# Kernel optimization log

Hardware: AMD Instinct MI355X
Metric: run time of the kernel (lower is better)

## Reference

```python
import jax, jax.numpy as jnp
import numpy as np

N_HEADS = 12
B, S, D = 2, 2048, 768
NEG = -1e9


def setup_inputs() -> dict:
    key = jax.random.key(0)
    ks = jax.random.split(key, 7)
    scale = 1.0 / np.sqrt(D)
    Q = jax.random.normal(ks[0], (B, S, D), jnp.float32)
    K = jax.random.normal(ks[1], (B, S, D), jnp.float32)
    V = jax.random.normal(ks[2], (B, S, D), jnp.float32)
    # causal mask, broadcastable over batch and heads; 0 entries are masked out
    mask = jnp.tril(jnp.ones((S, S), jnp.int32))[None, None, :, :]
    Wq = jax.random.normal(ks[3], (D, D), jnp.float32) * scale
    Wk = jax.random.normal(ks[4], (D, D), jnp.float32) * scale
    Wv = jax.random.normal(ks[5], (D, D), jnp.float32) * scale
    Wo = jax.random.normal(ks[6], (D, D), jnp.float32) * scale
    return {"Q": Q, "K": K, "V": V, "mask": mask,
            "Wq": Wq, "Wk": Wk, "Wv": Wv, "Wo": Wo}


def reference(Q, K, V, mask, Wq, Wk, Wv, Wo):
    b, s, d = Q.shape
    h = N_HEADS
    dk = d // h
    # projections (torch nn.Linear: x @ W.T), split heads -> (b, h, s, dk)
    q = (Q @ Wq.T).reshape(b, s, h, dk).transpose(0, 2, 1, 3)
    k = (K @ Wk.T).reshape(b, s, h, dk).transpose(0, 2, 1, 3)
    v = (V @ Wv.T).reshape(b, s, h, dk).transpose(0, 2, 1, 3)
    scores = jnp.einsum('bhqd,bhkd->bhqk', q, k) / jnp.sqrt(jnp.asarray(dk, q.dtype))
    scores = jnp.where(mask == 0, jnp.asarray(NEG, scores.dtype), scores)
    attn = jax.nn.softmax(scores, axis=-1)  # dropout p=0.0 -> identity
    ctx = jnp.einsum('bhqk,bhkd->bhqd', attn, v)
    ctx = ctx.transpose(0, 2, 1, 3).reshape(b, s, d)
    return ctx @ Wo.T
```

## Files before the change

### kernel.cpp

```cpp
#include <hip/hip_runtime.h>
#include <math.h>

#define NH     12
#define BB     2
#define SEQ    2048
#define DMODEL 768
#define DK     64

typedef __attribute__((ext_vector_type(8))) short short8;
typedef __attribute__((ext_vector_type(4))) short short4v;
typedef __attribute__((ext_vector_type(4))) float floatx4;

__device__ __forceinline__ unsigned short f2bf(float x) {
    unsigned u = __builtin_bit_cast(unsigned, x);
    u = (u + 0x7fffu + ((u >> 16) & 1u)) >> 16;
    return (unsigned short)u;
}
__device__ __forceinline__ unsigned short f2bf_fast(float x) {
    unsigned u = __builtin_bit_cast(unsigned, x);
    return (unsigned short)((u + 0x8000u) >> 16);
}
__device__ __forceinline__ float bf2f(unsigned short h) {
    unsigned u = ((unsigned)h) << 16;
    return __builtin_bit_cast(float, u);
}

__device__ __forceinline__ void gld_lds16(const ushort* gptr, ushort* lptr) {
    __builtin_amdgcn_global_load_lds(
        (const __attribute__((address_space(1))) unsigned int*)(const void*)gptr,
        (__attribute__((address_space(3))) unsigned int*)(void*)lptr,
        16, 0, 0);
}

__device__ __forceinline__ short4v shfl8(short4v v, int src) {
    int2 t = __builtin_bit_cast(int2, v);
    t.x = __shfl(t.x, src);
    t.y = __shfl(t.y, src);
    return __builtin_bit_cast(short4v, t);
}

#define SI (BB * SEQ * DMODEL)
#define SW (DMODEL * DMODEL)

__global__ __launch_bounds__(256) void cast_w(
    const float* __restrict__ Wq, const float* __restrict__ Wk,
    const float* __restrict__ Wv, const float* __restrict__ Wo,
    ushort* oWq, ushort* oWk, ushort* oWv, ushort* oWo, int* counter) {
    if (blockIdx.x == 0 && threadIdx.x == 0) *counter = 0;
    long i = (long)(blockIdx.x * 256 + threadIdx.x) * 4;
    const float* src; ushort* dst; long off;
    if      (i < 1L * SW) { src = Wq; dst = oWq; off = i; }
    else if (i < 2L * SW) { src = Wk; dst = oWk; off = i - 1L * SW; }
    else if (i < 3L * SW) { src = Wv; dst = oWv; off = i - 2L * SW; }
    else                  { src = Wo; dst = oWo; off = i - 3L * SW; }
    float4 v = *(const float4*)(src + off);
    ushort4 o;
    o.x = f2bf(v.x); o.y = f2bf(v.y); o.z = f2bf(v.z); o.w = f2bf(v.w);
    *(ushort4*)(dst + off) = o;
}

#define GTS (128 * 32)

template<int MODE, bool AF32>
__device__ __forceinline__ void gemm_body(ushort* __restrict__ Sbase,
                                          const void* __restrict__ Av,
                                          const ushort* __restrict__ W,
                                          float* __restrict__ outF,
                                          ushort* __restrict__ outH,
                                          float scale) {
    const int n0 = blockIdx.x * 128;
    const int m0 = blockIdx.y * 128;
    const int tid  = threadIdx.x;
    const int lane = tid & 63;
    const int wv   = tid >> 6;
    const int l15  = lane & 15;
    const int quad = lane >> 4;
    const int wm = (wv >> 1) * 64;
    const int wn = (wv & 1) * 64;

    const int srow = tid >> 2;
    const int sch  = tid & 3;
    const int schx = sch ^ ((srow >> 1) & 3);
    const int sw2  = (l15 >> 1) & 3;

    const ushort* Ab = (const ushort*)Av;
    const float*  Af = (const float*)Av;

    floatx4 acc[4][4];
    #pragma unroll
    for (int i = 0; i < 4; ++i)
        #pragma unroll
        for (int j = 0; j < 4; ++j) acc[i][j] = (floatx4)0.f;

    float4 ar0[2], ar1[2];
    #pragma unroll
    for (int it = 0; it < 2; ++it) {
        const int r = srow + it * 64;
        if (AF32) {
            const float* p = Af + (size_t)(m0 + r) * DMODEL + schx * 8;
            ar0[it] = *(const float4*)p;
            ar1[it] = *(const float4*)(p + 4);
        } else {
            gld_lds16(Ab + (size_t)(m0 + r) * DMODEL + schx * 8, Sbase + r * 32 + sch * 8);
        }
        gld_lds16(W + (size_t)(n0 + r) * DMODEL + schx * 8, Sbase + GTS + r * 32 + sch * 8);
    }
    if (AF32) {
        #pragma unroll
        for (int it = 0; it < 2; ++it) {
            const int r = srow + it * 64;
            short8 s8;
            s8[0] = (short)f2bf_fast(ar0[it].x); s8[1] = (short)f2bf_fast(ar0[it].y);
            s8[2] = (short)f2bf_fast(ar0[it].z); s8[3] = (short)f2bf_fast(ar0[it].w);
            s8[4] = (short)f2bf_fast(ar1[it].x); s8[5] = (short)f2bf_fast(ar1[it].y);
            s8[6] = (short)f2bf_fast(ar1[it].z); s8[7] = (short)f2bf_fast(ar1[it].w);
            *(short8*)(Sbase + r * 32 + sch * 8) = s8;
        }
    }

    const int NS = DMODEL / 32;
    for (int t = 0; t < NS; ++t) {
        __syncthreads();
        const int bi = (t + 1) & 1;
        ushort* SbufN = Sbase + bi * 2 * GTS;
        if (t + 1 < NS) {
            const int k0 = (t + 1) * 32;
            #pragma unroll
            for (int it = 0; it < 2; ++it) {
                const int r = srow + it * 64;
                if (AF32) {
                    const float* p = Af + (size_t)(m0 + r) * DMODEL + k0 + schx * 8;
                    ar0[it] = *(const float4*)p;
                    ar1[it] = *(const float4*)(p + 4);
                } else {
                    gld_lds16(Ab + (size_t)(m0 + r) * DMODEL + k0 + schx * 8, SbufN + r * 32 + sch * 8);
                }
                gld_lds16(W + (size_t)(n0 + r) * DMODEL + k0 + schx * 8, SbufN + GTS + r * 32 + sch * 8);
            }
        }
        const ushort* As  = Sbase + (t & 1) * 2 * GTS;
        const ushort* Ws2 = As + GTS;
        short8 af[4], bf[4];
        #pragma unroll
        for (int mi = 0; mi < 4; ++mi)
            af[mi] = *(const short8*)&As[(wm + mi * 16 + l15) * 32 + ((quad ^ sw2) * 8)];
        #pragma unroll
        for (int ni = 0; ni < 4; ++ni)
            bf[ni] = *(const short8*)&Ws2[(wn + ni * 16 + l15) * 32 + ((quad ^ sw2) * 8)];
        #pragma unroll
        for (int mi = 0; mi < 4; ++mi)
            #pragma unroll
            for (int ni = 0; ni < 4; ++ni) {
                if (MODE == 2)
                    acc[mi][ni] = __builtin_amdgcn_mfma_f32_16x16x32_bf16(bf[ni], af[mi], acc[mi][ni], 0, 0, 0);
                else
                    acc[mi][ni] = __builtin_amdgcn_mfma_f32_16x16x32_bf16(af[mi], bf[ni], acc[mi][ni], 0, 0, 0);
            }
        if (AF32 && t + 1 < NS) {
            #pragma unroll
            for (int it = 0; it < 2; ++it) {
                const int r = srow + it * 64;
                short8 s8;
                s8[0] = (short)f2bf_fast(ar0[it].x); s8[1] = (short)f2bf_fast(ar0[it].y);
                s8[2] = (short)f2bf_fast(ar0[it].z); s8[3] = (short)f2bf_fast(ar0[it].w);
                s8[4] = (short)f2bf_fast(ar1[it].x); s8[5] = (short)f2bf_fast(ar1[it].y);
                s8[6] = (short)f2bf_fast(ar1[it].z); s8[7] = (short)f2bf_fast(ar1[it].w);
                *(short8*)(SbufN + r * 32 + sch * 8) = s8;
            }
        }
    }

    #pragma unroll
    for (int mi = 0; mi < 4; ++mi)
        #pragma unroll
        for (int ni = 0; ni < 4; ++ni)
            #pragma unroll
            for (int r = 0; r < 4; ++r) {
                const float v = acc[mi][ni][r] * scale;
                if (MODE == 2) {
                    const int m = m0 + wm + mi * 16 + l15;
                    const int n = n0 + wn + ni * 16 + quad * 4 + r;
                    const int b = m >> 11, s = m & (SEQ - 1);
                    const int h = n >> 6,  dk = n & 63;
                    outH[(((size_t)b * NH + h) * DK + dk) * SEQ + s] = f2bf(v);
                } else {
                    const int m = m0 + wm + mi * 16 + quad * 4 + r;
                    const int n = n0 + wn + ni * 16 + l15;
                    if (MODE == 0) {
                        outF[(size_t)m * DMODEL + n] = v;
                    } else {
                        const int b = m >> 11, s = m & (SEQ - 1);
                        const int h = n >> 6,  dk = n & 63;
                        outH[(((size_t)b * NH + h) * SEQ + s) * DK + dk] = f2bf(v);
                    }
                }
            }
}

#define QSCALE (0.125f * 1.44269504088896f)

__global__ __launch_bounds__(256) void gemm_qkv(
    const float* Q, const float* K, const float* V,
    const ushort* Wqb, const ushort* Wkb, const ushort* Wvb,
    ushort* qh, ushort* kh, ushort* vhT) {
    __shared__ __align__(16) ushort S[2 * 2 * GTS];
    const int z = blockIdx.z;
    if (z == 0)      gemm_body<1, true>(S, Q, Wqb, nullptr, qh,  QSCALE);
    else if (z == 1) gemm_body<1, true>(S, K, Wkb, nullptr, kh,  1.0f);
    else             gemm_body<2, true>(S, V, Wvb, nullptr, vhT, 1.0f);
}

__global__ __launch_bounds__(256) void gemm_out(const ushort* A, const ushort* W, float* out) {
    __shared__ __align__(16) ushort S[2 * 2 * GTS];
    gemm_body<0, false>(S, A, W, out, nullptr, 1.0f);
}

#define NIT   (24 * 72)
#define MBIAS -20.0f
__device__ const int d_offs[17] = {0,1,2,4,6,9,12,16,20,25,30,36,42,49,56,64,72};

__global__ __launch_bounds__(256, 4) void flash_p1(const ushort* __restrict__ qh,
                                                   const ushort* __restrict__ kh,
                                                   const ushort* __restrict__ vhT,
                                                   ushort* __restrict__ ctx,
                                                   ushort* __restrict__ Opart,
                                                   float* __restrict__ lpart,
                                                   int* __restrict__ counter) {
    const int tid  = threadIdx.x;
    const int lane = tid & 63;
    const int wv   = tid >> 6;
    const int l15  = lane & 15;
    const int quad = lane >> 4;

    __shared__ __align__(16) ushort KV[2][2][64 * 64];
    __shared__ int wshare;

    const int srow = tid >> 3;
    const int sch  = tid & 7;
    const int schx = sch ^ (srow & 7);
    const int swq  = l15 & 7;

    const int srcA = l15 + 32 * (quad & 1);
    const int srcB = srcA + 16;
    const bool hiq = (quad >> 1) != 0;

    for (;;) {
        if (tid == 0) wshare = atomicAdd(counter, 1);
        __syncthreads();
        const int w = wshare;
        if (w >= NIT) break;
        const int bh = w / 72;
        const int r72 = w - bh * 72;
        int Q = 0;
        #pragma unroll
        for (int q = 0; q < 16; ++q) if (r72 >= d_offs[q + 1]) Q = q + 1;
        const int s  = r72 - d_offs[Q];
        const int ns = (Q >> 1) + 1;
        const int b  = bh / NH, h = bh % NH;
        const int qbase = Q * 128;
        const int k_lo = 4 * s;
        const int k_hi = min(4 * s + 3, 2 * Q + 1);

        const ushort* kbase = kh  + (size_t)bh * SEQ * DK;
        const ushort* vbase = vhT + (size_t)bh * DK * SEQ;

        short8 qf[2][2];
        #pragma unroll
        for (int qs = 0; qs < 2; ++qs) {
            const ushort* qp = qh + ((size_t)bh * SEQ + qbase + wv * 32 + qs * 16 + l15) * DK;
            qf[qs][0] = *(const short8*)(qp + quad * 8);
            qf[qs][1] = *(const short8*)(qp + 32 + quad * 8);
        }

        {
            const int k0 = k_lo * 64;
            gld_lds16(kbase + (size_t)(k0 + srow) * DK + schx * 8,        &KV[0][0][srow * 64 + sch * 8]);
            gld_lds16(kbase + (size_t)(k0 + srow + 32) * DK + schx * 8,   &KV[0][0][(srow + 32) * 64 + sch * 8]);
            gld_lds16(vbase + (size_t)srow * SEQ + k0 + schx * 8,         &KV[0][1][srow * 64 + sch * 8]);
            gld_lds16(vbase + (size_t)(srow + 32) * SEQ + k0 + schx * 8,  &KV[0][1][(srow + 32) * 64 + sch * 8]);
        }

        float l_s[2] = {0.f, 0.f};
        floatx4 o_acc[2][4];
        #pragma unroll
        for (int qs = 0; qs < 2; ++qs)
            #pragma unroll
            for (int d = 0; d < 4; ++d) o_acc[qs][d] = (floatx4)0.f;

        for (int kt = k_lo; kt <= k_hi; ++kt) {
            __syncthreads();
            if (kt < k_hi) {
                const int k0 = (kt + 1) * 64;
                const int bi = (kt + 1 - k_lo) & 1;
                gld_lds16(kbase + (size_t)(k0 + srow) * DK + schx * 8,        &KV[bi][0][srow * 64 + sch * 8]);
                gld_lds16(kbase + (size_t)(k0 + srow + 32) * DK + schx * 8,   &KV[bi][0][(srow + 32) * 64 + sch * 8]);
                gld_lds16(vbase + (size_t)srow * SEQ + k0 + schx * 8,         &KV[bi][1][srow * 64 + sch * 8]);
                gld_lds16(vbase + (size_t)(srow + 32) * SEQ + k0 + schx * 8,  &KV[bi][1][(srow + 32) * 64 + sch * 8]);
            }
            const int cb = (kt - k_lo) & 1;
            const ushort* Ks  = KV[cb][0];
            const ushort* Vts = KV[cb][1];
            const bool diag = (kt >= 2 * Q);

            #pragma unroll
            for (int qs = 0; qs < 2; ++qs) {
                floatx4 s_acc[4];
                #pragma unroll
                for (int nt = 0; nt < 4; ++nt) s_acc[nt] = (floatx4)(MBIAS);
                #pragma unroll
                for (int kc = 0; kc < 2; ++kc)
                    #pragma unroll
                    for (int nt = 0; nt < 4; ++nt) {
                        short8 kf = *(const short8*)&Ks[(nt * 16 + l15) * 64 + (((kc * 4 + quad) ^ swq) * 8)];
                        s_acc[nt] = __builtin_amdgcn_mfma_f32_16x16x32_bf16(kf, qf[qs][kc], s_acc[nt], 0, 0, 0);
                    }

                if (diag) {
                    const int qg = qbase + wv * 32 + qs * 16 + l15;
                    #pragma unroll
                    for (int nt = 0; nt < 4; ++nt)
                        #pragma unroll
                        for (int rr = 0; rr < 4; ++rr)
                            if (kt * 64 + nt * 16 + quad * 4 + rr > qg) s_acc[nt][rr] = -1.0e30f;
                }

                short4v packed[4];
                #pragma unroll
                for (int nt = 0; nt < 4; ++nt)
                    #pragma unroll
                    for (int rr = 0; rr < 4; ++rr) {
                        const float p = exp2f(s_acc[nt][rr]);
                        l_s[qs] += p;
                        packed[nt][rr] = (short)f2bf_fast(p);
                    }

                #pragma unroll
                for (int kc = 0; kc < 2; ++kc) {
                    short4v a0 = shfl8(packed[2 * kc],     srcA);
                    short4v a1 = shfl8(packed[2 * kc + 1], srcA);
                    short4v b0 = shfl8(packed[2 * kc],     srcB);
                    short4v b1 = shfl8(packed[2 * kc + 1], srcB);
                    short4v lo = hiq ? a1 : a0;
                    short4v hi = hiq ? b1 : b0;
                    short8 pf;
                    pf[0] = lo[0]; pf[1] = lo[1]; pf[2] = lo[2]; pf[3] = lo[3];
                    pf[4] = hi[0]; pf[5] = hi[1]; pf[6] = hi[2]; pf[7] = hi[3];
                    #pragma unroll
                    for (int dkt = 0; dkt < 4; ++dkt) {
                        short8 vf = *(const short8*)&Vts[(dkt * 16 + l15) * 64 + (((kc * 4 + quad) ^ swq) * 8)];
                        o_acc[qs][dkt] = __builtin_amdgcn_mfma_f32_16x16x32_bf16(pf, vf, o_acc[qs][dkt], 0, 0, 0);
                    }
                }
            }
        }

        #pragma unroll
        for (int qs = 0; qs < 2; ++qs) {
            l_s[qs] += __shfl_xor(l_s[qs], 16);
            l_s[qs] += __shfl_xor(l_s[qs], 32);
        }

        if (ns == 1) {
            #pragma unroll
            for (int qs = 0; qs < 2; ++qs)
                #pragma unroll
                for (int rr = 0; rr < 4; ++rr) {
                    const float lr = __shfl(l_s[qs], quad * 20 + rr);
                    const float inv = 1.f / lr;
                    const int sg = qbase + wv * 32 + qs * 16 + quad * 4 + rr;
                    #pragma unroll
                    for (int dkt = 0; dkt < 4; ++dkt) {
                        const int d = h * DK + dkt * 16 + l15;
                        ctx[((size_t)b * SEQ + sg) * DMODEL + d] = f2bf(o_acc[qs][dkt][rr] * inv);
                    }
                }
        } else {
            const int pid = bh * 70 + (d_offs[Q] - 2) + s;
            ushort* op = Opart + (size_t)pid * (128 * 64);
            #pragma unroll
            for (int qs = 0; qs < 2; ++qs) {
                #pragma unroll
                for (int rr = 0; rr < 4; ++rr) {
                    const int row = wv * 32 + qs * 16 + quad * 4 + rr;
                    #pragma unroll
                    for (int dkt = 0; dkt < 4; ++dkt)
                        op[row * 64 + dkt * 16 + l15] = f2bf(o_acc[qs][dkt][rr]);
                }
                if (quad == 0)
                    lpart[(size_t)pid * 128 + wv * 32 + qs * 16 + l15] = l_s[qs];
            }
        }
    }
}

__global__ __launch_bounds__(256) void flash_combine(const ushort* __restrict__ Opart,
                                                     const float* __restrict__ lpart,
                                                     ushort* __restrict__ ctx) {
    const int bh = blockIdx.x / 14;
    const int Q  = 2 + blockIdx.x % 14;
    const int ns = (Q >> 1) + 1;
    const int pbase = bh * 70 + (d_offs[Q] - 2);
    const int b = bh / NH, h = bh % NH;
    const int t = threadIdx.x;
    const int row = t >> 1;
    const int c0  = (t & 1) * 32;

    float lt = 0.f;
    for (int s2 = 0; s2 < ns; ++s2) lt += lpart[(size_t)(pbase + s2) * 128 + row];
    const float inv = 1.f / lt;

    float acc[32];
    #pragma unroll
    for (int j = 0; j < 32; ++j) acc[j] = 0.f;
    for (int s2 = 0; s2 < ns; ++s2) {
        const ushort* op = Opart + (size_t)(pbase + s2) * (128 * 64) + row * 64 + c0;
        #pragma unroll
        for (int j = 0; j < 32; j += 8) {
            short8 v = *(const short8*)(op + j);
            #pragma unroll
            for (int e = 0; e < 8; ++e) acc[j + e] += bf2f((unsigned short)v[e]);
        }
    }
    ushort* dst = ctx + ((size_t)b * SEQ + Q * 128 + row) * DMODEL + h * DK + c0;
    #pragma unroll
    for (int j = 0; j < 32; j += 8) {
        short8 o;
        #pragma unroll
        for (int e = 0; e < 8; ++e) o[e] = (short)f2bf(acc[j + e] * inv);
        *(short8*)(dst + j) = o;
    }
}

extern "C" void kernel_launch(void* const* d_in, const int* in_sizes, int n_in,
                              void* d_out, int out_size, void* d_ws, size_t ws_size,
                              hipStream_t stream) {
    const float* Q  = (const float*)d_in[0];
    const float* K  = (const float*)d_in[1];
    const float* V  = (const float*)d_in[2];
    const float* Wq = (const float*)d_in[4];
    const float* Wk = (const float*)d_in[5];
    const float* Wv = (const float*)d_in[6];
    const float* Wo = (const float*)d_in[7];

    char* ws = (char*)d_ws;
    const size_t SZ_IN = (size_t)SI * 2;
    const size_t SZ_W  = (size_t)SW * 2;
    ushort* Wqb   = (ushort*)(ws);
    ushort* Wkb   = (ushort*)(ws + SZ_W);
    ushort* Wvb   = (ushort*)(ws + 2 * SZ_W);
    ushort* Wob   = (ushort*)(ws + 3 * SZ_W);
    ushort* qh    = (ushort*)(ws + 4 * SZ_W);
    ushort* kh    = (ushort*)(ws + 4 * SZ_W + SZ_IN);
    ushort* vhT   = (ushort*)(ws + 4 * SZ_W + 2 * SZ_IN);
    ushort* ctx   = (ushort*)(ws + 4 * SZ_W + 3 * SZ_IN);
    ushort* Opart = (ushort*)(ws + 4 * SZ_W + 4 * SZ_IN);
    float*  lpart = (float*) (ws + 4 * SZ_W + 4 * SZ_IN + (size_t)1680 * 8192 * 2);
    int*    ctr   = (int*)   (ws + 4 * SZ_W + 4 * SZ_IN + (size_t)1680 * 8192 * 2
                                 + (size_t)1680 * 128 * 4);

    dim3 blk(256);
    cast_w<<<dim3(4 * SW / 1024), blk, 0, stream>>>(Wq, Wk, Wv, Wo,
                                                    Wqb, Wkb, Wvb, Wob, ctr);
    gemm_qkv<<<dim3(6, 32, 3), blk, 0, stream>>>(Q, K, V, Wqb, Wkb, Wvb, qh, kh, vhT);
    flash_p1<<<dim3(768), blk, 0, stream>>>(qh, kh, vhT, ctx, Opart, lpart, ctr);
    flash_combine<<<dim3(24 * 14), blk, 0, stream>>>(Opart, lpart, ctx);
    gemm_out<<<dim3(6, 32), blk, 0, stream>>>(ctx, Wob, (float*)d_out);
}
```

Baseline: 221.2 us.

## Retile output GEMM, swizzle GEMM blocks, prefetch work items in persistent flash kernel

The GEMM body is templated on the M tile size, so the output projection now runs 64-row tiles with twice as many workgroups. Both GEMMs remap block indices with a swizzle to group blocks that share operands, aiming at better cache reuse. The flash attention kernel now launches 1024 persistent blocks. Each block takes its first work item from its block index, and the atomic fetch for the next item is issued before the current one is processed, which takes one barrier off the critical path. The softmax row sum is split into four partial accumulators to shorten the dependency chain, at the cost of more blocks and slightly different summation order.

```diff
diff --git a/kernel.cpp b/kernel.cpp
--- a/kernel.cpp
+++ b/kernel.cpp
@@ -42,11 +42,13 @@
 #define SI (BB * SEQ * DMODEL)
 #define SW (DMODEL * DMODEL)
 
+#define P1_BLOCKS 1024
+
 __global__ __launch_bounds__(256) void cast_w(
     const float* __restrict__ Wq, const float* __restrict__ Wk,
     const float* __restrict__ Wv, const float* __restrict__ Wo,
     ushort* oWq, ushort* oWk, ushort* oWv, ushort* oWo, int* counter) {
-    if (blockIdx.x == 0 && threadIdx.x == 0) *counter = 0;
+    if (blockIdx.x == 0 && threadIdx.x == 0) *counter = P1_BLOCKS;
     long i = (long)(blockIdx.x * 256 + threadIdx.x) * 4;
     const float* src; ushort* dst; long off;
     if      (i < 1L * SW) { src = Wq; dst = oWq; off = i; }
@@ -59,23 +61,30 @@
     *(ushort4*)(dst + off) = o;
 }
 
-#define GTS (128 * 32)
-
-template<int MODE, bool AF32>
+template<int MODE, bool AF32, int TM>
 __device__ __forceinline__ void gemm_body(ushort* __restrict__ Sbase,
                                           const void* __restrict__ Av,
                                           const ushort* __restrict__ W,
                                           float* __restrict__ outF,
                                           ushort* __restrict__ outH,
                                           float scale) {
-    const int n0 = blockIdx.x * 128;
-    const int m0 = blockIdx.y * 128;
+    constexpr int ATS = TM * 32;
+    constexpr int BST = ATS + 128 * 32;
+    constexpr int MI  = TM / 32;
+    constexpr int AIT = TM / 64;
+    constexpr int NWG = (TM == 128) ? 192 : 384;
+
+    const int lin = blockIdx.y * 6 + blockIdx.x;
+    const int swz = (lin & 7) * (NWG / 8) + (lin >> 3);
+    const int n0 = (swz % 6) * 128;
+    const int m0 = (swz / 6) * TM;
+
     const int tid  = threadIdx.x;
     const int lane = tid & 63;
     const int wv   = tid >> 6;
     const int l15  = lane & 15;
     const int quad = lane >> 4;
-    const int wm = (wv >> 1) * 64;
+    const int wm = (wv >> 1) * (TM / 2);
     const int wn = (wv & 1) * 64;
 
     const int srow = tid >> 2;
@@ -86,15 +95,15 @@
     const ushort* Ab = (const ushort*)Av;
     const float*  Af = (const float*)Av;
 
-    floatx4 acc[4][4];
-    #pragma unroll
-    for (int i = 0; i < 4; ++i)
+    floatx4 acc[MI][4];
+    #pragma unroll
+    for (int i = 0; i < MI; ++i)
         #pragma unroll
         for (int j = 0; j < 4; ++j) acc[i][j] = (floatx4)0.f;
 
     float4 ar0[2], ar1[2];
     #pragma unroll
-    for (int it = 0; it < 2; ++it) {
+    for (int it = 0; it < AIT; ++it) {
         const int r = srow + it * 64;
         if (AF32) {
             const float* p = Af + (size_t)(m0 + r) * DMODEL + schx * 8;
@@ -103,11 +112,15 @@
         } else {
             gld_lds16(Ab + (size_t)(m0 + r) * DMODEL + schx * 8, Sbase + r * 32 + sch * 8);
         }
-        gld_lds16(W + (size_t)(n0 + r) * DMODEL + schx * 8, Sbase + GTS + r * 32 + sch * 8);
+    }
+    #pragma unroll
+    for (int it = 0; it < 2; ++it) {
+        const int r = srow + it * 64;
+        gld_lds16(W + (size_t)(n0 + r) * DMODEL + schx * 8, Sbase + ATS + r * 32 + sch * 8);
     }
     if (AF32) {
         #pragma unroll
-        for (int it = 0; it < 2; ++it) {
+        for (int it = 0; it < AIT; ++it) {
             const int r = srow + it * 64;
             short8 s8;
             s8[0] = (short)f2bf_fast(ar0[it].x); s8[1] = (short)f2bf_fast(ar0[it].y);
@@ -122,11 +135,11 @@
     for (int t = 0; t < NS; ++t) {
         __syncthreads();
         const int bi = (t + 1) & 1;
-        ushort* SbufN = Sbase + bi * 2 * GTS;
+        ushort* SbufN = Sbase + bi * BST;
         if (t + 1 < NS) {
             const int k0 = (t + 1) * 32;
             #pragma unroll
-            for (int it = 0; it < 2; ++it) {
+            for (int it = 0; it < AIT; ++it) {
                 const int r = srow + it * 64;
                 if (AF32) {
                     const float* p = Af + (size_t)(m0 + r) * DMODEL + k0 + schx * 8;
@@ -135,20 +148,24 @@
                 } else {
                     gld_lds16(Ab + (size_t)(m0 + r) * DMODEL + k0 + schx * 8, SbufN + r * 32 + sch * 8);
                 }
-                gld_lds16(W + (size_t)(n0 + r) * DMODEL + k0 + schx * 8, SbufN + GTS + r * 32 + sch * 8);
-            }
-        }
-        const ushort* As  = Sbase + (t & 1) * 2 * GTS;
-        const ushort* Ws2 = As + GTS;
-        short8 af[4], bf[4];
-        #pragma unroll
-        for (int mi = 0; mi < 4; ++mi)
+            }
+            #pragma unroll
+            for (int it = 0; it < 2; ++it) {
+                const int r = srow + it * 64;
+                gld_lds16(W + (size_t)(n0 + r) * DMODEL + k0 + schx * 8, SbufN + ATS + r * 32 + sch * 8);
+            }
+        }
+        const ushort* As  = Sbase + (t & 1) * BST;
+        const ushort* Ws2 = As + ATS;
+        short8 af[MI], bf[4];
+        #pragma unroll
+        for (int mi = 0; mi < MI; ++mi)
             af[mi] = *(const short8*)&As[(wm + mi * 16 + l15) * 32 + ((quad ^ sw2) * 8)];
         #pragma unroll
         for (int ni = 0; ni < 4; ++ni)
             bf[ni] = *(const short8*)&Ws2[(wn + ni * 16 + l15) * 32 + ((quad ^ sw2) * 8)];
         #pragma unroll
-        for (int mi = 0; mi < 4; ++mi)
+        for (int mi = 0; mi < MI; ++mi)
             #pragma unroll
             for (int ni = 0; ni < 4; ++ni) {
                 if (MODE == 2)
@@ -158,7 +175,7 @@
             }
         if (AF32 && t + 1 < NS) {
             #pragma unroll
-            for (int it = 0; it < 2; ++it) {
+            for (int it = 0; it < AIT; ++it) {
                 const int r = srow + it * 64;
                 short8 s8;
                 s8[0] = (short)f2bf_fast(ar0[it].x); s8[1] = (short)f2bf_fast(ar0[it].y);
@@ -171,7 +188,7 @@
     }
 
     #pragma unroll
-    for (int mi = 0; mi < 4; ++mi)
+    for (int mi = 0; mi < MI; ++mi)
         #pragma unroll
         for (int ni = 0; ni < 4; ++ni)
             #pragma unroll
@@ -203,16 +220,16 @@
     const float* Q, const float* K, const float* V,
     const ushort* Wqb, const ushort* Wkb, const ushort* Wvb,
     ushort* qh, ushort* kh, ushort* vhT) {
-    __shared__ __align__(16) ushort S[2 * 2 * GTS];
+    __shared__ __align__(16) ushort S[2 * (128 * 32 + 128 * 32)];
     const int z = blockIdx.z;
-    if (z == 0)      gemm_body<1, true>(S, Q, Wqb, nullptr, qh,  QSCALE);
-    else if (z == 1) gemm_body<1, true>(S, K, Wkb, nullptr, kh,  1.0f);
-    else             gemm_body<2, true>(S, V, Wvb, nullptr, vhT, 1.0f);
+    if (z == 0)      gemm_body<1, true, 128>(S, Q, Wqb, nullptr, qh,  QSCALE);
+    else if (z == 1) gemm_body<1, true, 128>(S, K, Wkb, nullptr, kh,  1.0f);
+    else             gemm_body<2, true, 128>(S, V, Wvb, nullptr, vhT, 1.0f);
 }
 
 __global__ __launch_bounds__(256) void gemm_out(const ushort* A, const ushort* W, float* out) {
-    __shared__ __align__(16) ushort S[2 * 2 * GTS];
-    gemm_body<0, false>(S, A, W, out, nullptr, 1.0f);
+    __shared__ __align__(16) ushort S[2 * (64 * 32 + 128 * 32)];
+    gemm_body<0, false, 64>(S, A, W, out, nullptr, 1.0f);
 }
 
 #define NIT   (24 * 72)
@@ -244,11 +261,10 @@
     const int srcB = srcA + 16;
     const bool hiq = (quad >> 1) != 0;
 
+    int w = blockIdx.x;
     for (;;) {
+        if (w >= NIT) break;
         if (tid == 0) wshare = atomicAdd(counter, 1);
-        __syncthreads();
-        const int w = wshare;
-        if (w >= NIT) break;
         const int bh = w / 72;
         const int r72 = w - bh * 72;
         int Q = 0;
@@ -324,15 +340,20 @@
                             if (kt * 64 + nt * 16 + quad * 4 + rr > qg) s_acc[nt][rr] = -1.0e30f;
                 }
 
+                float lp0 = 0.f, lp1 = 0.f, lp2 = 0.f, lp3 = 0.f;
                 short4v packed[4];
                 #pragma unroll
                 for (int nt = 0; nt < 4; ++nt)
                     #pragma unroll
                     for (int rr = 0; rr < 4; ++rr) {
                         const float p = exp2f(s_acc[nt][rr]);
-                        l_s[qs] += p;
+                        if      (rr == 0) lp0 += p;
+                        else if (rr == 1) lp1 += p;
+                        else if (rr == 2) lp2 += p;
+                        else              lp3 += p;
                         packed[nt][rr] = (short)f2bf_fast(p);
                     }
+                l_s[qs] += (lp0 + lp1) + (lp2 + lp3);
 
                 #pragma unroll
                 for (int kc = 0; kc < 2; ++kc) {
@@ -390,6 +411,9 @@
                     lpart[(size_t)pid * 128 + wv * 32 + qs * 16 + l15] = l_s[qs];
             }
         }
+
+        w = wshare;
+        __syncthreads();
     }
 }
 
@@ -462,7 +486,7 @@
     cast_w<<<dim3(4 * SW / 1024), blk, 0, stream>>>(Wq, Wk, Wv, Wo,
                                                     Wqb, Wkb, Wvb, Wob, ctr);
     gemm_qkv<<<dim3(6, 32, 3), blk, 0, stream>>>(Q, K, V, Wqb, Wkb, Wvb, qh, kh, vhT);
-    flash_p1<<<dim3(768), blk, 0, stream>>>(qh, kh, vhT, ctx, Opart, lpart, ctr);
+    flash_p1<<<dim3(P1_BLOCKS), blk, 0, stream>>>(qh, kh, vhT, ctx, Opart, lpart, ctr);
     flash_combine<<<dim3(24 * 14), blk, 0, stream>>>(Opart, lpart, ctx);
-    gemm_out<<<dim3(6, 32), blk, 0, stream>>>(ctx, Wob, (float*)d_out);
-}
+    gemm_out<<<dim3(6, 64), blk, 0, stream>>>(ctx, Wob, (float*)d_out);
+}
```

Measured after the change: 211.2 us. 1.05x faster.
